# Kernel tuning notes

Measured on AMD Instinct MI355X. Metric: run time of the kernel, lower is better.

The kernel has to match this reference:

```python
import jax, jax.numpy as jnp
import numpy as np

B, N, K = 2, 2048, 30          # batch, residues, neighbors
DN, DE, L = 256, 128, 3        # dim_nodes, dim_edges, num_layers
NF, EF = 12, 28                # raw node / edge feature dims
EPS = 1e-6


def _gather(h, idx):
    # h: [B,N,D], idx: [B,N,K] -> [B,N,K,D]
    b, n, k = idx.shape
    d = h.shape[-1]
    return jnp.take_along_axis(h, idx.reshape(b, n * k, 1), axis=1).reshape(b, n, k, d)


def _nrm(v):
    return v / (jnp.linalg.norm(v, axis=-1, keepdims=True) + EPS)


def _forward(X, C, Wn, bn, We, be, Wm1, bm1, Wm2, bm2, Wue1, bue1, Wue2, bue2):
    mask_i = (C > 0).astype(X.dtype)                      # [B,N]
    Nat, CA, Cat, Oat = X[..., 0, :], X[..., 1, :], X[..., 2, :], X[..., 3, :]

    # local residue frames via Gram-Schmidt on (N, CA, C)
    u = _nrm(Cat - CA)
    v0 = Nat - CA
    v = _nrm(v0 - jnp.sum(v0 * u, -1, keepdims=True) * u)
    w = jnp.cross(u, v)
    R = jnp.stack([u, v, w], axis=-1)                     # [B,N,3,3]

    # node features: internal coords (unit bond vectors + log lengths)
    def bond_feat(bv):
        return jnp.concatenate([_nrm(bv), jnp.log(jnp.linalg.norm(bv, axis=-1, keepdims=True) + EPS)], -1)
    node_feat = jnp.concatenate([bond_feat(CA - Nat), bond_feat(Cat - CA), bond_feat(Oat - Cat)], -1)  # [B,N,12]
    node_h = (node_feat @ Wn + bn) * mask_i[..., None]

    # kNN graph on centroid distances (graph_distance_atom_type=-1)
    Xc = X.mean(axis=2)                                   # [B,N,3]
    D2 = jnp.sum((Xc[:, :, None] - Xc[:, None, :]) ** 2, -1)  # [B,N,N]
    BIG = 1e9
    D2 = D2 + BIG * (1.0 - mask_i)[:, None, :] + BIG * jnp.eye(N, dtype=X.dtype)[None]
    _, edge_idx = jax.lax.top_k(-D2, K)                   # [B,N,K]

    mask_j = _gather(mask_i[..., None], edge_idx)[..., 0]
    mask_ij = mask_i[..., None] * mask_j                  # [B,N,K]

    # edge features: RBF distances + local-frame direction + relative rotation
    xj = _gather(Xc, edge_idx)
    d = xj - Xc[:, :, None]                               # [B,N,K,3]
    dist = jnp.linalg.norm(d, axis=-1)
    local = jnp.einsum('bndc,bnkd->bnkc', R, d)           # R_i^T d
    dirv = local / (dist[..., None] + EPS)
    Rj = _gather(R.reshape(B, N, 9), edge_idx).reshape(B, N, K, 3, 3)
    Rrel = jnp.einsum('bnde,bnkdf->bnkef', R, Rj).reshape(B, N, K, 9)  # R_i^T R_j
    centers = jnp.linspace(0.0, 20.0, 16)
    sigma = 20.0 / 16.0
    rbf = jnp.exp(-(((dist[..., None] - centers) / sigma) ** 2))       # [B,N,K,16]
    edge_h = (jnp.concatenate([rbf, dirv, Rrel], -1) @ We + be) * mask_ij[..., None]

    # GNN message passing: gather -> MLP -> masked mean scatter, + edge update
    denom = jnp.sum(mask_ij, -1, keepdims=True) + EPS     # [B,N,1]
    for l in range(L):
        hj = _gather(node_h, edge_idx)                    # [B,N,K,DN]
        hi = jnp.broadcast_to(node_h[:, :, None], hj.shape)
        mi = jnp.concatenate([hi, hj, edge_h], -1)        # [B,N,K,2*DN+DE]
        m = jax.nn.softplus(mi @ Wm1[l] + bm1[l]) @ Wm2[l] + bm2[l]
        m = m * mask_ij[..., None]
        node_h = (node_h + m.sum(axis=2) / denom) * mask_i[..., None]
        e = jax.nn.softplus(mi @ Wue1[l] + bue1[l]) @ Wue2[l] + bue2[l]
        edge_h = (edge_h + e) * mask_ij[..., None]

    return node_h, edge_h, edge_idx, mask_i, mask_ij


def setup_inputs() -> dict:
    key = jax.random.key(0)
    ks = jax.random.split(key, 10)
    s = lambda i, shp: jax.random.normal(ks[i], shp, jnp.float32) * 0.05
    M = 2 * DN + DE
    inp = {
        'X': jax.random.normal(ks[0], (B, N, 4, 3), jnp.float32),
        'C': jax.random.randint(ks[1], (B, N), 0, 4),
        'Wn': s(2, (NF, DN)), 'bn': jnp.zeros((DN,), jnp.float32),
        'We': s(3, (EF, DE)), 'be': jnp.zeros((DE,), jnp.float32),
        'Wm1': s(4, (L, M, DN)), 'bm1': jnp.zeros((L, DN), jnp.float32),
        'Wm2': s(5, (L, DN, DN)), 'bm2': jnp.zeros((L, DN), jnp.float32),
        'Wue1': s(6, (L, M, DE)), 'bue1': jnp.zeros((L, DE), jnp.float32),
        'Wue2': s(7, (L, DE, DE)), 'bue2': jnp.zeros((L, DE), jnp.float32),
    }
    return inp


def reference(X, C, Wn, bn, We, be, Wm1, bm1, Wm2, bm2, Wue1, bue1, Wue2, bue2):
    return _forward(X, C, Wn, bn, We, be, Wm1, bm1, Wm2, bm2, Wue1, bue1, Wue2, bue2)
```

## Files before the change

kernel.cpp:

```cpp
#include <hip/hip_runtime.h>
#include <math.h>

#define Bdim 2
#define Nn   2048
#define Kn   30
#define KP   32
#define DNc  256
#define DEc  128
#define NODES (Bdim*Nn)
#define EDGES (Bdim*Nn*Kn)
#define RPAD  (NODES*KP)
#define EPSF 1e-6f

#define BK 64
#define LDA (BK+8)
#define LDP 136

typedef __attribute__((ext_vector_type(8))) short short8;
typedef __attribute__((ext_vector_type(4))) short sh4;
typedef __attribute__((ext_vector_type(4))) float floatx4;

__device__ __forceinline__ float softplusf(float x){
    float e = __expf(-fabsf(x));
    return fmaxf(x, 0.f) + __logf(1.f + e);
}

__device__ __forceinline__ unsigned short f2bf(float x){
    union { float f; unsigned u; } v; v.f = x;
    unsigned r = v.u + 0x7fff + ((v.u >> 16) & 1);
    return (unsigned short)(r >> 16);
}
__device__ __forceinline__ float bf2f(unsigned short h){
    union { unsigned u; float f; } v; v.u = ((unsigned)h) << 16;
    return v.f;
}

__global__ __launch_bounds__(256) void k_geom(
    const float* __restrict__ X, const int* __restrict__ C,
    float* __restrict__ Xc, float* __restrict__ Rm,
    float* __restrict__ feat, float* __restrict__ mask_out)
{
    int id = blockIdx.x*256 + threadIdx.x;
    if (id >= NODES) return;
    float a[4][3];
    #pragma unroll
    for (int t=0;t<4;++t)
        #pragma unroll
        for (int d=0;d<3;++d) a[t][d] = X[id*12 + t*3 + d];
    #pragma unroll
    for (int d=0; d<3; ++d){
        float s = __fadd_rn(__fadd_rn(__fadd_rn(a[0][d],a[1][d]),a[2][d]),a[3][d]);
        Xc[id*3+d] = __fmul_rn(s, 0.25f);
    }
    mask_out[id] = (C[id] > 0) ? 1.f : 0.f;

    float u[3], v[3], w[3], b2[3], v0[3], vv[3];
    #pragma unroll
    for (int d=0;d<3;++d) b2[d] = a[2][d]-a[1][d];
    float n2 = sqrtf(b2[0]*b2[0]+b2[1]*b2[1]+b2[2]*b2[2]);
    #pragma unroll
    for (int d=0;d<3;++d) u[d] = b2[d]/(n2+EPSF);
    #pragma unroll
    for (int d=0;d<3;++d) v0[d] = a[0][d]-a[1][d];
    float dt = v0[0]*u[0]+v0[1]*u[1]+v0[2]*u[2];
    #pragma unroll
    for (int d=0;d<3;++d) vv[d] = v0[d] - dt*u[d];
    float nv = sqrtf(vv[0]*vv[0]+vv[1]*vv[1]+vv[2]*vv[2]);
    #pragma unroll
    for (int d=0;d<3;++d) v[d] = vv[d]/(nv+EPSF);
    w[0] = u[1]*v[2]-u[2]*v[1];
    w[1] = u[2]*v[0]-u[0]*v[2];
    w[2] = u[0]*v[1]-u[1]*v[0];
    #pragma unroll
    for (int d=0;d<3;++d){
        Rm[id*9 + d*3 + 0] = u[d];
        Rm[id*9 + d*3 + 1] = v[d];
        Rm[id*9 + d*3 + 2] = w[d];
    }
    float bonds[3][3];
    #pragma unroll
    for (int d=0;d<3;++d){
        bonds[0][d] = a[1][d]-a[0][d];
        bonds[1][d] = b2[d];
        bonds[2][d] = a[3][d]-a[2][d];
    }
    #pragma unroll
    for (int bi=0;bi<3;++bi){
        float nb = sqrtf(bonds[bi][0]*bonds[bi][0]+bonds[bi][1]*bonds[bi][1]+bonds[bi][2]*bonds[bi][2]);
        #pragma unroll
        for (int d=0;d<3;++d) feat[id*12 + bi*4 + d] = bonds[bi][d]/(nb+EPSF);
        feat[id*12 + bi*4 + 3] = logf(nb+EPSF);
    }
}

__global__ __launch_bounds__(256) void k_nodeh(
    const float* __restrict__ feat, const float* __restrict__ Wn,
    const float* __restrict__ bn, const int* __restrict__ C,
    float* __restrict__ node_h, unsigned short* __restrict__ node_bf)
{
    int nid = blockIdx.x;
    int c   = threadIdx.x;
    __shared__ float f[12];
    if (c < 12) f[c] = feat[nid*12 + c];
    __syncthreads();
    float acc = bn[c];
    #pragma unroll
    for (int k=0;k<12;++k) acc += f[k]*Wn[k*DNc + c];
    float mask = (C[nid] > 0) ? 1.f : 0.f;
    float r = acc*mask;
    node_h[nid*DNc + c] = r;
    node_bf[nid*DNc + c] = f2bf(r);
}

__global__ __launch_bounds__(256) void k_knn(
    const float* __restrict__ Xc, const int* __restrict__ C,
    int* __restrict__ eidx, float* __restrict__ eidx_f)
{
    __shared__ float sx[Nn], sy[Nn], sz[Nn], sadd[Nn];
    int tid  = threadIdx.x;
    int lane = tid & 63, wave = tid >> 6;
    int node0 = blockIdx.x*4;
    int base  = (node0 >> 11) << 11;
    for (int j=tid; j<Nn; j+=256){
        int gj = base + j;
        sx[j] = Xc[gj*3+0]; sy[j] = Xc[gj*3+1]; sz[j] = Xc[gj*3+2];
        sadd[j] = (C[gj] > 0) ? 0.f : 1e9f;
    }
    __syncthreads();

    int node = node0 + wave;
    int iloc = node & (Nn-1);
    float xi = sx[iloc], yi = sy[iloc], zi = sz[iloc];

    unsigned long long kreg[32];
    unsigned long long gm[8];
    #pragma unroll
    for (int t=0; t<32; ++t){
        int j = lane + t*64;
        float dx = __fsub_rn(xi, sx[j]);
        float dy = __fsub_rn(yi, sy[j]);
        float dz = __fsub_rn(zi, sz[j]);
        float vv = __fadd_rn(__fadd_rn(__fmul_rn(dx,dx),__fmul_rn(dy,dy)),__fmul_rn(dz,dz));
        vv = __fadd_rn(vv, sadd[j]);
        if (j == iloc) vv = __fadd_rn(vv, 1e9f);
        union { float f; unsigned u; } cv; cv.f = vv;
        kreg[t] = (((unsigned long long)cv.u) << 11) | (unsigned)j;
    }
    #pragma unroll
    for (int g=0; g<8; ++g){
        unsigned long long a = kreg[4*g+0], b = kreg[4*g+1];
        unsigned long long c = kreg[4*g+2], d = kreg[4*g+3];
        unsigned long long m1 = a<b?a:b, m2 = c<d?c:d;
        gm[g] = m1<m2?m1:m2;
    }
    unsigned long long m = gm[0]; int marg = 0;
    #pragma unroll
    for (int g=1; g<8; ++g) if (gm[g] < m){ m = gm[g]; marg = g; }

    for (int kk=0; kk<Kn; ++kk){
        unsigned long long best = m;
        #pragma unroll
        for (int d=1; d<64; d<<=1){
            unsigned long long o = __shfl_xor(best, d, 64);
            if (o < best) best = o;
        }
        if (lane == 0){
            int j = (int)(best & 2047ull);
            eidx  [(size_t)node*Kn + kk] = j;
            eidx_f[(size_t)node*Kn + kk] = (float)j;
        }
        if (m == best){
            #pragma unroll
            for (int g=0; g<8; ++g){
                if (marg == g){
                    #pragma unroll
                    for (int t=0; t<4; ++t)
                        if (kreg[4*g+t] == best) kreg[4*g+t] = ~0ull;
                    unsigned long long a = kreg[4*g+0], b = kreg[4*g+1];
                    unsigned long long c = kreg[4*g+2], d = kreg[4*g+3];
                    unsigned long long m1 = a<b?a:b, m2 = c<d?c:d;
                    gm[g] = m1<m2?m1:m2;
                }
            }
            m = gm[0]; marg = 0;
            #pragma unroll
            for (int g=1; g<8; ++g) if (gm[g] < m){ m = gm[g]; marg = g; }
        }
    }
}

__global__ __launch_bounds__(256) void k_edge(
    const float* __restrict__ Xc, const float* __restrict__ Rm,
    const int* __restrict__ eidx, const int* __restrict__ C,
    const float* __restrict__ We, const float* __restrict__ be,
    unsigned short* __restrict__ edge_pad, float* __restrict__ mask_ij_out,
    float* __restrict__ mask_pad, int* __restrict__ jg_pad,
    float* __restrict__ cnt)
{
    __shared__ float sWe[28*128];
    __shared__ float sbe[128];
    __shared__ float sfeat[30][28];
    __shared__ float smij[30];
    __shared__ float sRi[9];
    int nid = blockIdx.x;
    int b   = nid >> 11;
    int tid = threadIdx.x;
    for (int idx=tid; idx<28*128; idx+=256) sWe[idx] = We[idx];
    if (tid < 128) sbe[tid] = be[tid];
    if (tid < 9)   sRi[tid] = Rm[nid*9 + tid];
    __syncthreads();
    if (tid < KP){
        if (tid < Kn){
            int e  = nid*Kn + tid;
            int j  = eidx[e];
            int jb = (b<<11) + j;
            jg_pad[nid*KP + tid] = jb;
            float d0 = Xc[jb*3+0]-Xc[nid*3+0];
            float d1 = Xc[jb*3+1]-Xc[nid*3+1];
            float d2v= Xc[jb*3+2]-Xc[nid*3+2];
            float dist = sqrtf(d0*d0+d1*d1+d2v*d2v);
            float mij = (C[nid] > 0 && C[jb] > 0) ? 1.f : 0.f;
            smij[tid] = mij;
            mask_ij_out[e] = mij;
            mask_pad[nid*KP + tid] = mij;
            #pragma unroll
            for (int c=0; c<16; ++c){
                float ctr = (20.f/15.f)*(float)c;
                float t = (dist - ctr)*(1.f/1.25f);
                sfeat[tid][c] = expf(-t*t);
            }
            #pragma unroll
            for (int cc=0; cc<3; ++cc){
                float loc = sRi[0*3+cc]*d0 + sRi[1*3+cc]*d1 + sRi[2*3+cc]*d2v;
                sfeat[tid][16+cc] = loc/(dist+EPSF);
            }
            float rj[9];
            #pragma unroll
            for (int q=0;q<9;++q) rj[q] = Rm[jb*9+q];
            #pragma unroll
            for (int ee=0; ee<3; ++ee)
                #pragma unroll
                for (int ff=0; ff<3; ++ff)
                    sfeat[tid][19+ee*3+ff] = sRi[0+ee]*rj[0+ff] + sRi[3+ee]*rj[3+ff] + sRi[6+ee]*rj[6+ff];
        } else {
            jg_pad[nid*KP + tid] = nid;
            mask_pad[nid*KP + tid] = 0.f;
        }
    }
    __syncthreads();
    if (tid == 0){
        float c = 0.f;
        #pragma unroll
        for (int k=0;k<Kn;++k) c += smij[k];
        cnt[nid] = c;
    }
    int c  = tid & 127;
    int eg = tid >> 7;
    for (int k=eg; k<KP; k+=2){
        if (k < Kn){
            float acc = sbe[c];
            #pragma unroll
            for (int f=0; f<28; ++f) acc += sfeat[k][f]*sWe[f*128 + c];
            edge_pad[(size_t)(nid*KP + k)*DEc + c] = f2bf(acc * smij[k]);
        } else {
            edge_pad[(size_t)(nid*KP + k)*DEc + c] = 0;
        }
    }
}

__global__ __launch_bounds__(256) void k_pack_pqw(
    const float* __restrict__ Wm1, const float* __restrict__ Wue1,
    unsigned short* __restrict__ wPQw)
{
    int id = blockIdx.x*256 + threadIdx.x;
    if (id >= 3*768*256) return;
    int l = id / (768*256);
    int rem = id % (768*256);
    int n = rem >> 8, k = rem & 255;
    int c = (n < 384) ? n : n - 384;
    int r = (n < 384) ? k : 256 + k;
    float v = (c < 256) ? Wm1[((size_t)l*640 + r)*256 + c]
                        : Wue1[((size_t)l*640 + r)*128 + (c-256)];
    wPQw[id] = f2bf(v);
}

__global__ __launch_bounds__(256) void k_pack_ew(
    const float* __restrict__ Wm1, const float* __restrict__ Wue1,
    unsigned short* __restrict__ wEw)
{
    int id = blockIdx.x*256 + threadIdx.x;
    if (id >= 3*384*128) return;
    int l = id / (384*128);
    int rem = id % (384*128);
    int n = rem >> 7, k = rem & 127;
    int r = 512 + k;
    float v = (n < 256) ? Wm1[((size_t)l*640 + r)*256 + n]
                        : Wue1[((size_t)l*640 + r)*128 + (n-256)];
    wEw[id] = f2bf(v);
}

__global__ __launch_bounds__(256) void k_pack_ue2(
    const float* __restrict__ Wue2, unsigned short* __restrict__ wUe2w)
{
    int id = blockIdx.x*256 + threadIdx.x;
    if (id >= 3*128*128) return;
    int l = id / (128*128);
    int rem = id % (128*128);
    int n = rem >> 7, k = rem & 127;
    wUe2w[id] = f2bf(Wue2[((size_t)l*128 + k)*128 + n]);
}

__global__ __launch_bounds__(256) void k_pack_m2(
    const float* __restrict__ Wm2, unsigned short* __restrict__ wM2w)
{
    int id = blockIdx.x*256 + threadIdx.x;
    if (id >= 3*256*256) return;
    int l = id / (256*256);
    int rem = id % (256*256);
    int n = rem >> 8, k = rem & 255;
    wM2w[id] = f2bf(Wm2[((size_t)l*256 + k)*256 + n]);
}

template<int NR>
__device__ __forceinline__ void stage_tile_t(
    const unsigned short* __restrict__ gbase, int ldg, int k0,
    unsigned short* lds, int tid)
{
    #pragma unroll
    for (int it=0; it<NR/32; ++it){
        int idx = it*256 + tid;
        int row = idx >> 3;
        int ke  = (idx & 7) * 8;
        const float4* src = (const float4*)(gbase + (size_t)row*ldg + k0 + ke);
        *(float4*)(&lds[row*LDA + ke]) = *src;
    }
}

template<int TI, int TJ>
__device__ __forceinline__ void mma_tile_t(
    const unsigned short* Als, const unsigned short* Bls,
    int wm, int wn, int lane, floatx4 acc[TI][TJ])
{
    #pragma unroll
    for (int s=0; s<2; ++s){
        short8 af[TI], bf[TJ];
        int kidx = s*32 + (lane>>4)*8;
        #pragma unroll
        for (int t=0;t<TI;++t){
            int row = wm*(TI*16) + t*16 + (lane&15);
            af[t] = *(const short8*)(&Als[row*LDA + kidx]);
        }
        #pragma unroll
        for (int t=0;t<TJ;++t){
            int col = wn*(TJ*16) + t*16 + (lane&15);
            bf[t] = *(const short8*)(&Bls[col*LDA + kidx]);
        }
        #pragma unroll
        for (int i=0;i<TI;++i)
            #pragma unroll
            for (int j=0;j<TJ;++j)
                acc[i][j] = __builtin_amdgcn_mfma_f32_16x16x32_bf16(af[i], bf[j], acc[i][j], 0,0,0);
    }
}

__device__ __forceinline__ void mma_tileA_lp(
    const unsigned short* Atile, const unsigned short* Bls,
    int k0, int wm, int wn, int lane, floatx4 acc[4][4])
{
    #pragma unroll
    for (int s=0; s<2; ++s){
        short8 af[4], bf[4];
        int kloc = s*32 + (lane>>4)*8;
        #pragma unroll
        for (int t=0;t<4;++t){
            int row = wm*64 + t*16 + (lane&15);
            af[t] = *(const short8*)(&Atile[row*LDP + k0 + kloc]);
            int col = wn*64 + t*16 + (lane&15);
            bf[t] = *(const short8*)(&Bls[col*LDA + kloc]);
        }
        #pragma unroll
        for (int i=0;i<4;++i)
            #pragma unroll
            for (int j=0;j<4;++j)
                acc[i][j] = __builtin_amdgcn_mfma_f32_16x16x32_bf16(af[i], bf[j], acc[i][j], 0,0,0);
    }
}

__global__ __launch_bounds__(256) void k_pq(
    const unsigned short* __restrict__ A, const unsigned short* __restrict__ Bw,
    unsigned short* __restrict__ PQbf,
    const float* __restrict__ bm1l, const float* __restrict__ bue1l)
{
    __shared__ __align__(16) unsigned short smem[(64+128)*LDA];
    unsigned short* Als = smem;
    unsigned short* Bls = smem + 64*LDA;
    unsigned short* tile = smem;
    int tid = threadIdx.x;
    int lane = tid & 63, wave = tid >> 6;
    int wm = wave >> 1, wn = wave & 1;
    const unsigned short* Ab = A + (size_t)blockIdx.x*64*256;
    const unsigned short* Bb = Bw + (size_t)blockIdx.y*128*256;
    floatx4 acc[2][4];
    #pragma unroll
    for (int i=0;i<2;++i)
        #pragma unroll
        for (int j=0;j<4;++j) acc[i][j] = (floatx4){0.f,0.f,0.f,0.f};
    for (int k0=0; k0<256; k0+=BK){
        stage_tile_t<64>(Ab, 256, k0, Als, tid);
        stage_tile_t<128>(Bb, 256, k0, Bls, tid);
        __syncthreads();
        mma_tile_t<2,4>(Als, Bls, wm, wn, lane, acc);
        __syncthreads();
    }
    int quad = lane >> 4, cl = lane & 15;
    #pragma unroll
    for (int i=0;i<2;++i){
        #pragma unroll
        for (int rg=0;rg<4;++rg){
            int rowl = wm*32 + i*16 + quad*4 + rg;
            #pragma unroll
            for (int j=0;j<4;++j){
                int coll = wn*64 + j*16 + cl;
                int col  = blockIdx.y*128 + coll;
                float biasv = 0.f;
                if (col < 256)       biasv = bm1l[col];
                else if (col < 384)  biasv = bue1l[col-256];
                tile[rowl*LDP + coll] = f2bf(acc[i][j][rg] + biasv);
            }
        }
    }
    __syncthreads();
    {
        int rl = tid >> 2;
        int h  = tid & 3;
        unsigned short* dst = PQbf + (size_t)(blockIdx.x*64 + rl)*768 + blockIdx.y*128 + h*32;
        #pragma unroll
        for (int q=0; q<4; ++q)
            *(short8*)(dst + q*8) = *(const short8*)(&tile[rl*LDP + h*32 + q*8]);
    }
}

__global__ __launch_bounds__(256) void k_h1s(
    const unsigned short* __restrict__ Apad, const unsigned short* __restrict__ Bw,
    const unsigned short* __restrict__ PQbf, const int* __restrict__ jg_pad,
    const float* __restrict__ mask_pad,
    unsigned short* __restrict__ Sout)
{
    __shared__ __align__(16) unsigned short smem[2*128*LDA];
    __shared__ float smask[128];
    unsigned short* Als = smem;
    unsigned short* Bls = smem + 128*LDA;
    unsigned short* pqT = smem;

    int tid = threadIdx.x;
    int lane = tid & 63, wave = tid >> 6;
    int wm = wave >> 1, wn = wave & 1;
    int colblk = blockIdx.y;

    const unsigned short* Ab = Apad + (size_t)blockIdx.x*128*128;
    const unsigned short* Bb = Bw + (size_t)colblk*128*128;
    floatx4 acc[4][4];
    #pragma unroll
    for (int i=0;i<4;++i)
        #pragma unroll
        for (int j=0;j<4;++j) acc[i][j] = (floatx4){0.f,0.f,0.f,0.f};
    for (int k0=0; k0<128; k0+=BK){
        stage_tile_t<128>(Ab, 128, k0, Als, tid);
        stage_tile_t<128>(Bb, 128, k0, Bls, tid);
        __syncthreads();
        mma_tile_t<4,4>(Als, Bls, wm, wn, lane, acc);
        __syncthreads();
    }

    {
        int colbase = colblk*128;
        #pragma unroll
        for (int it=0; it<2; ++it){
            int w    = it*256 + tid;
            int rq   = w & 31;
            int c8   = w >> 5;
            int row0 = rq*4;
            int r0   = blockIdx.x*128 + row0;
            int ni   = r0 >> 5;
            int4 jg4 = *(const int4*)&jg_pad[r0];
            int colg = colbase + c8*8;
            short8 pv = *(const short8*)(PQbf + (size_t)ni*768 + colg);
            short8 q0 = *(const short8*)(PQbf + (size_t)jg4.x*768 + 384 + colg);
            short8 q1 = *(const short8*)(PQbf + (size_t)jg4.y*768 + 384 + colg);
            short8 q2 = *(const short8*)(PQbf + (size_t)jg4.z*768 + 384 + colg);
            short8 q3 = *(const short8*)(PQbf + (size_t)jg4.w*768 + 384 + colg);
            #pragma unroll
            for (int q=0; q<8; ++q){
                float pf = bf2f((unsigned short)pv[q]);
                sh4 ov;
                ov[0] = (short)f2bf(pf + bf2f((unsigned short)q0[q]));
                ov[1] = (short)f2bf(pf + bf2f((unsigned short)q1[q]));
                ov[2] = (short)f2bf(pf + bf2f((unsigned short)q2[q]));
                ov[3] = (short)f2bf(pf + bf2f((unsigned short)q3[q]));
                *(sh4*)(&pqT[(c8*8 + q)*LDP + row0]) = ov;
            }
        }
        if (tid < 128) smask[tid] = mask_pad[blockIdx.x*128 + tid];
    }
    __syncthreads();

    int quad = lane >> 4, cl = lane & 15;
    float sumA[4] = {0.f,0.f,0.f,0.f};
    float sumB[4] = {0.f,0.f,0.f,0.f};
    #pragma unroll
    for (int i=0;i<4;++i){
        int rowl0 = wm*64 + i*16 + quad*4;
        float4 mk = *(const float4*)&smask[rowl0];
        float mkv[4] = {mk.x, mk.y, mk.z, mk.w};
        #pragma unroll
        for (int j=0;j<4;++j){
            int coll = wn*64 + j*16 + cl;
            sh4 pq4 = *(const sh4*)(&pqT[coll*LDP + rowl0]);
            #pragma unroll
            for (int rg=0; rg<4; ++rg){
                float v  = softplusf(acc[i][j][rg] + bf2f((unsigned short)pq4[rg]));
                float mv = mkv[rg]*v;
                if (i < 2) sumA[j] += mv; else sumB[j] += mv;
            }
        }
    }

    int nodeA = blockIdx.x*4 + wm*2;
    #pragma unroll
    for (int j=0;j<4;++j){
        float a = sumA[j];
        a += __shfl_xor(a, 16, 64);
        a += __shfl_xor(a, 32, 64);
        float b = sumB[j];
        b += __shfl_xor(b, 16, 64);
        b += __shfl_xor(b, 32, 64);
        int col = colblk*128 + wn*64 + j*16 + cl;
        if (quad == 0)      Sout[(size_t)nodeA*256 + col]     = f2bf(a);
        else if (quad == 1) Sout[(size_t)(nodeA+1)*256 + col] = f2bf(b);
    }
}

__global__ __launch_bounds__(256) void k_h1e(
    const unsigned short* __restrict__ Apad, const unsigned short* __restrict__ BwE,
    const unsigned short* __restrict__ BwU2,
    const unsigned short* __restrict__ PQbf, const int* __restrict__ jg_pad,
    const float* __restrict__ mask_pad, const float* __restrict__ bue2l,
    unsigned short* __restrict__ edge_pad, float* __restrict__ edge_f32,
    int last)
{
    __shared__ __align__(16) unsigned short smem[26624];
    unsigned short* Als  = smem;
    unsigned short* Bls  = smem + 128*LDA;
    unsigned short* tile = smem;
    unsigned short* B2   = smem + 128*LDP;

    int tid = threadIdx.x;
    int lane = tid & 63, wave = tid >> 6;
    int wm = wave >> 1, wn = wave & 1;

    const unsigned short* Ab = Apad + (size_t)blockIdx.x*128*128;
    floatx4 acc[4][4];
    #pragma unroll
    for (int i=0;i<4;++i)
        #pragma unroll
        for (int j=0;j<4;++j) acc[i][j] = (floatx4){0.f,0.f,0.f,0.f};
    for (int k0=0; k0<128; k0+=BK){
        stage_tile_t<128>(Ab, 128, k0, Als, tid);
        stage_tile_t<128>(BwE, 128, k0, Bls, tid);
        __syncthreads();
        mma_tile_t<4,4>(Als, Bls, wm, wn, lane, acc);
        __syncthreads();
    }

    stage_tile_t<128>(BwU2, 128, 0, B2, tid);

    {
        int rl = tid >> 1;
        int h  = tid & 1;
        int r  = blockIdx.x*128 + rl;
        int ni = r >> 5;
        int jg = jg_pad[r];
        int cb = 256 + h*64;
        const unsigned short* Pr = PQbf + (size_t)ni*768 + cb;
        const unsigned short* Qr = PQbf + (size_t)jg*768 + 384 + cb;
        #pragma unroll
        for (int q=0; q<8; ++q){
            short8 pv = *(const short8*)(Pr + q*8);
            short8 qv = *(const short8*)(Qr + q*8);
            short8 ov;
            #pragma unroll
            for (int z=0; z<8; ++z)
                ov[z] = (short)f2bf(bf2f((unsigned short)pv[z]) + bf2f((unsigned short)qv[z]));
            *(short8*)(&tile[rl*LDP + h*64 + q*8]) = ov;
        }
    }
    __syncthreads();

    int quad = lane >> 4, cl = lane & 15;
    #pragma unroll
    for (int i=0;i<4;++i){
        #pragma unroll
        for (int rg=0;rg<4;++rg){
            int rowl = wm*64 + i*16 + quad*4 + rg;
            #pragma unroll
            for (int j=0;j<4;++j){
                int coll = wn*64 + j*16 + cl;
                float pq = bf2f(tile[rowl*LDP + coll]);
                float v  = softplusf(acc[i][j][rg] + pq);
                tile[rowl*LDP + coll] = f2bf(v);
            }
        }
    }
    __syncthreads();

    floatx4 acc2[4][4];
    #pragma unroll
    for (int i=0;i<4;++i)
        #pragma unroll
        for (int j=0;j<4;++j) acc2[i][j] = (floatx4){0.f,0.f,0.f,0.f};
    mma_tileA_lp(tile, B2, 0, wm, wn, lane, acc2);
    __syncthreads();
    stage_tile_t<128>(BwU2, 128, 64, B2, tid);
    __syncthreads();
    mma_tileA_lp(tile, B2, 64, wm, wn, lane, acc2);
    __syncthreads();

    float* sbias = (float*)B2;
    #pragma unroll
    for (int i=0;i<4;++i){
        #pragma unroll
        for (int rg=0;rg<4;++rg){
            int rowl = wm*64 + i*16 + quad*4 + rg;
            #pragma unroll
            for (int j=0;j<4;++j){
                int coll = wn*64 + j*16 + cl;
                tile[rowl*LDP + coll] = f2bf(acc2[i][j][rg]);
            }
        }
    }
    if (tid < 128) sbias[tid] = bue2l[tid];
    __syncthreads();

    if (last){
        int c16  = lane & 31;
        int rsub = lane >> 5;
        #pragma unroll
        for (int step=0; step<16; ++step){
            int rowl = wave*32 + step*2 + rsub;
            int R = blockIdx.x*128 + rowl;
            int k = R & (KP-1);
            if (k < Kn){
                float mij = mask_pad[R];
                int node = R >> 5;
                int e = node*Kn + k;
                sh4 ov = *(const sh4*)(edge_pad + (size_t)R*128 + c16*4);
                sh4 av = *(const sh4*)(&tile[rowl*LDP + c16*4]);
                float4 bv = *(const float4*)(&sbias[c16*4]);
                float4 f;
                f.x = (bf2f((unsigned short)ov[0]) + bf2f((unsigned short)av[0]) + bv.x)*mij;
                f.y = (bf2f((unsigned short)ov[1]) + bf2f((unsigned short)av[1]) + bv.y)*mij;
                f.z = (bf2f((unsigned short)ov[2]) + bf2f((unsigned short)av[2]) + bv.z)*mij;
                f.w = (bf2f((unsigned short)ov[3]) + bf2f((unsigned short)av[3]) + bv.w)*mij;
                *(float4*)(edge_f32 + (size_t)e*128 + c16*4) = f;
            }
        }
    } else {
        int c8   = lane & 15;
        int rsub = lane >> 4;
        #pragma unroll
        for (int step=0; step<8; ++step){
            int rowl = wave*32 + step*4 + rsub;
            int R = blockIdx.x*128 + rowl;
            int k = R & (KP-1);
            if (k < Kn){
                float mij = mask_pad[R];
                unsigned short* ep = edge_pad + (size_t)R*128 + c8*8;
                short8 ov = *(const short8*)ep;
                short8 av = *(const short8*)(&tile[rowl*LDP + c8*8]);
                float4 b0 = *(const float4*)(&sbias[c8*8]);
                float4 b1 = *(const float4*)(&sbias[c8*8 + 4]);
                float nv[8];
                nv[0] = (bf2f((unsigned short)ov[0]) + bf2f((unsigned short)av[0]) + b0.x)*mij;
                nv[1] = (bf2f((unsigned short)ov[1]) + bf2f((unsigned short)av[1]) + b0.y)*mij;
                nv[2] = (bf2f((unsigned short)ov[2]) + bf2f((unsigned short)av[2]) + b0.z)*mij;
                nv[3] = (bf2f((unsigned short)ov[3]) + bf2f((unsigned short)av[3]) + b0.w)*mij;
                nv[4] = (bf2f((unsigned short)ov[4]) + bf2f((unsigned short)av[4]) + b1.x)*mij;
                nv[5] = (bf2f((unsigned short)ov[5]) + bf2f((unsigned short)av[5]) + b1.y)*mij;
                nv[6] = (bf2f((unsigned short)ov[6]) + bf2f((unsigned short)av[6]) + b1.z)*mij;
                nv[7] = (bf2f((unsigned short)ov[7]) + bf2f((unsigned short)av[7]) + b1.w)*mij;
                short8 sv;
                #pragma unroll
                for (int z=0; z<8; ++z) sv[z] = (short)f2bf(nv[z]);
                *(short8*)ep = sv;
            }
        }
    }
}

__global__ __launch_bounds__(256) void k_node_gemm(
    const unsigned short* __restrict__ S, const unsigned short* __restrict__ Bw,
    const float* __restrict__ bm2l, const float* __restrict__ cnt,
    const float* __restrict__ mask_i,
    float* __restrict__ node_h, unsigned short* __restrict__ node_bf)
{
    __shared__ __align__(16) unsigned short Als[64*LDA];
    __shared__ __align__(16) unsigned short Bls[64*LDA];
    int tid = threadIdx.x;
    int lane = tid & 63, wave = tid >> 6;
    int wm = wave >> 1, wn = wave & 1;
    const unsigned short* Ab = S + (size_t)blockIdx.x*64*256;
    const unsigned short* Bb = Bw + (size_t)blockIdx.y*64*256;
    floatx4 acc[2][2];
    #pragma unroll
    for (int i=0;i<2;++i)
        #pragma unroll
        for (int j=0;j<2;++j) acc[i][j] = (floatx4){0.f,0.f,0.f,0.f};
    for (int k0=0; k0<256; k0+=BK){
        stage_tile_t<64>(Ab, 256, k0, Als, tid);
        stage_tile_t<64>(Bb, 256, k0, Bls, tid);
        __syncthreads();
        mma_tile_t<2,2>(Als, Bls, wm, wn, lane, acc);
        __syncthreads();
    }
    int quad = lane >> 4, cl = lane & 15;
    #pragma unroll
    for (int i=0;i<2;++i){
        #pragma unroll
        for (int rg=0;rg<4;++rg){
            int nid = blockIdx.x*64 + wm*32 + i*16 + quad*4 + rg;
            float ct = cnt[nid];
            float mi = mask_i[nid];
            #pragma unroll
            for (int j=0;j<2;++j){
                int col = blockIdx.y*64 + wn*32 + j*16 + cl;
                float msum = acc[i][j][rg] + ct*bm2l[col];
                float nh = node_h[(size_t)nid*256 + col];
                float r = (nh + msum/(ct+EPSF))*mi;
                node_h[(size_t)nid*256 + col] = r;
                node_bf[(size_t)nid*256 + col] = f2bf(r);
            }
        }
    }
}

extern "C" void kernel_launch(void* const* d_in, const int* in_sizes, int n_in,
                              void* d_out, int out_size, void* d_ws, size_t ws_size,
                              hipStream_t stream)
{
    (void)in_sizes; (void)n_in; (void)out_size; (void)ws_size;
    const float* X   = (const float*)d_in[0];
    const int*   C   = (const int*)  d_in[1];
    const float* Wn  = (const float*)d_in[2];
    const float* bn  = (const float*)d_in[3];
    const float* We  = (const float*)d_in[4];
    const float* be  = (const float*)d_in[5];
    const float* Wm1 = (const float*)d_in[6];
    const float* bm1 = (const float*)d_in[7];
    const float* Wm2 = (const float*)d_in[8];
    const float* bm2 = (const float*)d_in[9];
    const float* Wue1= (const float*)d_in[10];
    const float* bue1= (const float*)d_in[11];
    const float* Wue2= (const float*)d_in[12];
    const float* bue2= (const float*)d_in[13];

    float* out       = (float*)d_out;
    float* out_node  = out;
    float* out_edge  = out + 1048576;
    float* out_eidxf = out + 16777216;
    float* out_maski = out + 16900096;
    float* out_maskij= out + 16904192;

    char* wsb = (char*)d_ws;
    size_t off = 0;
    float* wXc    = (float*)(wsb + off); off += (size_t)12288*4;
    float* wR     = (float*)(wsb + off); off += (size_t)36864*4;
    float* wF     = (float*)(wsb + off); off += (size_t)49152*4;
    int*   wEidx  = (int*)  (wsb + off); off += (size_t)EDGES*4;
    int*   wJgPad = (int*)  (wsb + off); off += (size_t)RPAD*4;
    float* wMaskP = (float*)(wsb + off); off += (size_t)RPAD*4;
    float* wCnt   = (float*)(wsb + off); off += (size_t)NODES*4;
    unsigned short* wPQ      = (unsigned short*)(wsb + off); off += (size_t)NODES*768*2;
    unsigned short* wS       = (unsigned short*)(wsb + off); off += (size_t)NODES*256*2;
    unsigned short* wNodeBf  = (unsigned short*)(wsb + off); off += (size_t)NODES*256*2;
    unsigned short* wEdgePad = (unsigned short*)(wsb + off); off += (size_t)RPAD*128*2;
    unsigned short* wPQw     = (unsigned short*)(wsb + off); off += (size_t)3*768*256*2;
    unsigned short* wEw      = (unsigned short*)(wsb + off); off += (size_t)3*384*128*2;
    unsigned short* wUe2w    = (unsigned short*)(wsb + off); off += (size_t)3*128*128*2;
    unsigned short* wM2w     = (unsigned short*)(wsb + off); off += (size_t)3*256*256*2;

    k_geom <<<16,    256, 0, stream>>>(X, C, wXc, wR, wF, out_maski);
    k_nodeh<<<NODES, 256, 0, stream>>>(wF, Wn, bn, C, out_node, wNodeBf);
    k_knn  <<<NODES/4, 256, 0, stream>>>(wXc, C, wEidx, out_eidxf);
    k_edge <<<NODES, 256, 0, stream>>>(wXc, wR, wEidx, C, We, be,
                                       wEdgePad, out_maskij, wMaskP, wJgPad, wCnt);

    k_pack_pqw<<<(3*768*256+255)/256, 256, 0, stream>>>(Wm1, Wue1, wPQw);
    k_pack_ew <<<(3*384*128+255)/256, 256, 0, stream>>>(Wm1, Wue1, wEw);
    k_pack_ue2<<<(3*128*128+255)/256, 256, 0, stream>>>(Wue2, wUe2w);
    k_pack_m2 <<<(3*256*256+255)/256, 256, 0, stream>>>(Wm2, wM2w);

    for (int l=0; l<3; ++l){
        k_pq<<<dim3(64,6), 256, 0, stream>>>(wNodeBf, wPQw + (size_t)l*768*256, wPQ,
                                             bm1 + l*256, bue1 + l*128);
        k_h1s<<<dim3(RPAD/128,2), 256, 0, stream>>>(
            wEdgePad, wEw + (size_t)l*384*128, wPQ, wJgPad, wMaskP, wS);
        k_h1e<<<RPAD/128, 256, 0, stream>>>(
            wEdgePad, wEw + (size_t)l*384*128 + (size_t)256*128,
            wUe2w + (size_t)l*128*128, wPQ, wJgPad, wMaskP, bue2 + l*128,
            wEdgePad, out_edge, (l==2) ? 1 : 0);
        k_node_gemm<<<dim3(NODES/64,4), 256, 0, stream>>>(
            wS, wM2w + (size_t)l*256*256, bm2 + l*256, wCnt, out_maski,
            out_node, wNodeBf);
    }
}
```

Before: 509.7 us.

## Split edge embedding into per-edge feature kernel and bf16 MFMA GEMM

```diff
diff --git a/kernel.cpp b/kernel.cpp
--- a/kernel.cpp
+++ b/kernel.cpp
@@ -14,6 +14,7 @@
 
 #define BK 64
 #define LDA (BK+8)
+#define LDA0 40
 #define LDP 136
 
 typedef __attribute__((ext_vector_type(8))) short short8;
@@ -189,83 +190,169 @@
     }
 }
 
-__global__ __launch_bounds__(256) void k_edge(
+__global__ __launch_bounds__(256) void k_edge_feat(
     const float* __restrict__ Xc, const float* __restrict__ Rm,
     const int* __restrict__ eidx, const int* __restrict__ C,
-    const float* __restrict__ We, const float* __restrict__ be,
-    unsigned short* __restrict__ edge_pad, float* __restrict__ mask_ij_out,
-    float* __restrict__ mask_pad, int* __restrict__ jg_pad,
-    float* __restrict__ cnt)
-{
-    __shared__ float sWe[28*128];
-    __shared__ float sbe[128];
-    __shared__ float sfeat[30][28];
-    __shared__ float smij[30];
-    __shared__ float sRi[9];
-    int nid = blockIdx.x;
+    unsigned short* __restrict__ featp,
+    float* __restrict__ mask_ij_out, float* __restrict__ mask_pad,
+    int* __restrict__ jg_pad, float* __restrict__ cnt)
+{
+    int r   = blockIdx.x*256 + threadIdx.x;
+    int nid = r >> 5;
+    int k   = r & 31;
     int b   = nid >> 11;
+    float mij = 0.f;
+    int   jb  = nid;
+    float f[28];
+    if (k < Kn){
+        int e = nid*Kn + k;
+        int j = eidx[e];
+        jb = (b<<11) + j;
+        mij = (C[nid] > 0 && C[jb] > 0) ? 1.f : 0.f;
+        mask_ij_out[e] = mij;
+        float xi0 = Xc[nid*3+0], xi1 = Xc[nid*3+1], xi2 = Xc[nid*3+2];
+        float d0  = Xc[jb*3+0]-xi0;
+        float d1  = Xc[jb*3+1]-xi1;
+        float d2v = Xc[jb*3+2]-xi2;
+        float dist = sqrtf(d0*d0 + d1*d1 + d2v*d2v);
+        float ri[9], rj[9];
+        #pragma unroll
+        for (int q=0;q<9;++q) ri[q] = Rm[nid*9+q];
+        #pragma unroll
+        for (int q=0;q<9;++q) rj[q] = Rm[jb*9+q];
+        #pragma unroll
+        for (int c=0; c<16; ++c){
+            float ctr = (20.f/15.f)*(float)c;
+            float t = (dist - ctr)*(1.f/1.25f);
+            f[c] = expf(-t*t);
+        }
+        #pragma unroll
+        for (int cc=0; cc<3; ++cc){
+            float loc = ri[0*3+cc]*d0 + ri[1*3+cc]*d1 + ri[2*3+cc]*d2v;
+            f[16+cc] = loc/(dist+EPSF);
+        }
+        #pragma unroll
+        for (int ee=0; ee<3; ++ee)
+            #pragma unroll
+            for (int ff=0; ff<3; ++ff)
+                f[19+ee*3+ff] = ri[0+ee]*rj[0+ff] + ri[3+ee]*rj[3+ff] + ri[6+ee]*rj[6+ff];
+    }
+    jg_pad[r]   = jb;
+    mask_pad[r] = mij;
+
+    unsigned long long bal = __ballot(mij > 0.f);
+    int lane = threadIdx.x & 63;
+    if (lane == 0)  cnt[r >> 5] = (float)__popcll(bal & 0xFFFFFFFFull);
+    if (lane == 32) cnt[r >> 5] = (float)__popcll(bal >> 32);
+
+    unsigned short ov[32];
+    #pragma unroll
+    for (int q=0;q<32;++q) ov[q] = 0;
+    if (k < Kn){
+        #pragma unroll
+        for (int q=0;q<28;++q) ov[q] = f2bf(f[q]);
+    }
+    unsigned short* dst = featp + (size_t)r*32;
+    #pragma unroll
+    for (int q=0; q<4; ++q){
+        short8 sv;
+        #pragma unroll
+        for (int z=0; z<8; ++z) sv[z] = (short)ov[q*8+z];
+        *(short8*)(dst + q*8) = sv;
+    }
+}
+
+__global__ __launch_bounds__(256) void k_edge0(
+    const unsigned short* __restrict__ featp, const unsigned short* __restrict__ Wp,
+    const float* __restrict__ be, const float* __restrict__ mask_pad,
+    unsigned short* __restrict__ edge_pad)
+{
+    __shared__ __align__(16) unsigned short smem[128*LDP];
+    __shared__ float smask[128];
+    unsigned short* Als  = smem;
+    unsigned short* Bls  = smem + 128*LDA0;
+    unsigned short* tile = smem;
+
     int tid = threadIdx.x;
-    for (int idx=tid; idx<28*128; idx+=256) sWe[idx] = We[idx];
-    if (tid < 128) sbe[tid] = be[tid];
-    if (tid < 9)   sRi[tid] = Rm[nid*9 + tid];
-    __syncthreads();
-    if (tid < KP){
-        if (tid < Kn){
-            int e  = nid*Kn + tid;
-            int j  = eidx[e];
-            int jb = (b<<11) + j;
-            jg_pad[nid*KP + tid] = jb;
-            float d0 = Xc[jb*3+0]-Xc[nid*3+0];
-            float d1 = Xc[jb*3+1]-Xc[nid*3+1];
-            float d2v= Xc[jb*3+2]-Xc[nid*3+2];
-            float dist = sqrtf(d0*d0+d1*d1+d2v*d2v);
-            float mij = (C[nid] > 0 && C[jb] > 0) ? 1.f : 0.f;
-            smij[tid] = mij;
-            mask_ij_out[e] = mij;
-            mask_pad[nid*KP + tid] = mij;
-            #pragma unroll
-            for (int c=0; c<16; ++c){
-                float ctr = (20.f/15.f)*(float)c;
-                float t = (dist - ctr)*(1.f/1.25f);
-                sfeat[tid][c] = expf(-t*t);
+    int lane = tid & 63, wave = tid >> 6;
+    int wm = wave >> 1, wn = wave & 1;
+
+    {
+        const unsigned short* Ab = featp + (size_t)blockIdx.x*128*32;
+        #pragma unroll
+        for (int it=0; it<2; ++it){
+            int idx = it*256 + tid;
+            int row = idx >> 2, q = idx & 3;
+            *(float4*)(&Als[row*LDA0 + q*8]) = *(const float4*)(Ab + row*32 + q*8);
+        }
+        if (tid < 128){
+            int row = tid;
+            *(float4*)(&Bls[row*LDA0 + 0])  = *(const float4*)(Wp + row*32 + 0);
+            *(float4*)(&Bls[row*LDA0 + 8])  = *(const float4*)(Wp + row*32 + 8);
+            *(float4*)(&Bls[row*LDA0 + 16]) = *(const float4*)(Wp + row*32 + 16);
+            *(float4*)(&Bls[row*LDA0 + 24]) = *(const float4*)(Wp + row*32 + 24);
+        } else {
+            smask[tid-128] = mask_pad[blockIdx.x*128 + (tid-128)];
+        }
+    }
+    __syncthreads();
+
+    floatx4 acc[4][4];
+    #pragma unroll
+    for (int i=0;i<4;++i)
+        #pragma unroll
+        for (int j=0;j<4;++j) acc[i][j] = (floatx4){0.f,0.f,0.f,0.f};
+    short8 af[4], bf[4];
+    int kidx = (lane>>4)*8;
+    #pragma unroll
+    for (int t=0;t<4;++t){
+        int row = wm*64 + t*16 + (lane&15);
+        af[t] = *(const short8*)(&Als[row*LDA0 + kidx]);
+        int col = wn*64 + t*16 + (lane&15);
+        bf[t] = *(const short8*)(&Bls[col*LDA0 + kidx]);
+    }
+    __syncthreads();
+    #pragma unroll
+    for (int i=0;i<4;++i)
+        #pragma unroll
+        for (int j=0;j<4;++j)
+            acc[i][j] = __builtin_amdgcn_mfma_f32_16x16x32_bf16(af[i], bf[j], acc[i][j], 0,0,0);
+
+    int quad = lane >> 4, cl = lane & 15;
+    float be_r[4];
+    #pragma unroll
+    for (int j=0;j<4;++j) be_r[j] = be[wn*64 + j*16 + cl];
+    #pragma unroll
+    for (int i=0;i<4;++i){
+        #pragma unroll
+        for (int rg=0;rg<4;++rg){
+            int rowl = wm*64 + i*16 + quad*4 + rg;
+            float mk = smask[rowl];
+            #pragma unroll
+            for (int j=0;j<4;++j){
+                int coll = wn*64 + j*16 + cl;
+                tile[rowl*LDP + coll] = f2bf((acc[i][j][rg] + be_r[j]) * mk);
             }
-            #pragma unroll
-            for (int cc=0; cc<3; ++cc){
-                float loc = sRi[0*3+cc]*d0 + sRi[1*3+cc]*d1 + sRi[2*3+cc]*d2v;
-                sfeat[tid][16+cc] = loc/(dist+EPSF);
-            }
-            float rj[9];
-            #pragma unroll
-            for (int q=0;q<9;++q) rj[q] = Rm[jb*9+q];
-            #pragma unroll
-            for (int ee=0; ee<3; ++ee)
-                #pragma unroll
-                for (int ff=0; ff<3; ++ff)
-                    sfeat[tid][19+ee*3+ff] = sRi[0+ee]*rj[0+ff] + sRi[3+ee]*rj[3+ff] + sRi[6+ee]*rj[6+ff];
-        } else {
-            jg_pad[nid*KP + tid] = nid;
-            mask_pad[nid*KP + tid] = 0.f;
-        }
-    }
-    __syncthreads();
-    if (tid == 0){
-        float c = 0.f;
-        #pragma unroll
-        for (int k=0;k<Kn;++k) c += smij[k];
-        cnt[nid] = c;
-    }
-    int c  = tid & 127;
-    int eg = tid >> 7;
-    for (int k=eg; k<KP; k+=2){
-        if (k < Kn){
-            float acc = sbe[c];
-            #pragma unroll
-            for (int f=0; f<28; ++f) acc += sfeat[k][f]*sWe[f*128 + c];
-            edge_pad[(size_t)(nid*KP + k)*DEc + c] = f2bf(acc * smij[k]);
-        } else {
-            edge_pad[(size_t)(nid*KP + k)*DEc + c] = 0;
-        }
-    }
+        }
+    }
+    __syncthreads();
+    {
+        int rl = tid >> 1;
+        int h  = tid & 1;
+        unsigned short* dst = edge_pad + (size_t)(blockIdx.x*128 + rl)*128 + h*64;
+        #pragma unroll
+        for (int q=0; q<8; ++q)
+            *(short8*)(dst + q*8) = *(const short8*)(&tile[rl*LDP + h*64 + q*8]);
+    }
+}
+
+__global__ __launch_bounds__(256) void k_pack_we0(
+    const float* __restrict__ We, unsigned short* __restrict__ Wp)
+{
+    int id = blockIdx.x*256 + threadIdx.x;
+    if (id >= 128*32) return;
+    int n = id >> 5, kk = id & 31;
+    Wp[id] = (kk < 28) ? f2bf(We[kk*128 + n]) : 0;
 }
 
 __global__ __launch_bounds__(256) void k_pack_pqw(
@@ -783,6 +870,8 @@
     unsigned short* wS       = (unsigned short*)(wsb + off); off += (size_t)NODES*256*2;
     unsigned short* wNodeBf  = (unsigned short*)(wsb + off); off += (size_t)NODES*256*2;
     unsigned short* wEdgePad = (unsigned short*)(wsb + off); off += (size_t)RPAD*128*2;
+    unsigned short* wFeatP   = (unsigned short*)(wsb + off); off += (size_t)RPAD*32*2;
+    unsigned short* wWe0     = (unsigned short*)(wsb + off); off += (size_t)128*32*2;
     unsigned short* wPQw     = (unsigned short*)(wsb + off); off += (size_t)3*768*256*2;
     unsigned short* wEw      = (unsigned short*)(wsb + off); off += (size_t)3*384*128*2;
     unsigned short* wUe2w    = (unsigned short*)(wsb + off); off += (size_t)3*128*128*2;
@@ -791,8 +880,11 @@
     k_geom <<<16,    256, 0, stream>>>(X, C, wXc, wR, wF, out_maski);
     k_nodeh<<<NODES, 256, 0, stream>>>(wF, Wn, bn, C, out_node, wNodeBf);
     k_knn  <<<NODES/4, 256, 0, stream>>>(wXc, C, wEidx, out_eidxf);
-    k_edge <<<NODES, 256, 0, stream>>>(wXc, wR, wEidx, C, We, be,
-                                       wEdgePad, out_maskij, wMaskP, wJgPad, wCnt);
+
+    k_pack_we0<<<16, 256, 0, stream>>>(We, wWe0);
+    k_edge_feat<<<RPAD/256, 256, 0, stream>>>(wXc, wR, wEidx, C, wFeatP,
+                                              out_maskij, wMaskP, wJgPad, wCnt);
+    k_edge0<<<RPAD/128, 256, 0, stream>>>(wFeatP, wWe0, be, wMaskP, wEdgePad);
 
     k_pack_pqw<<<(3*768*256+255)/256, 256, 0, stream>>>(Wm1, Wue1, wPQw);
     k_pack_ew <<<(3*384*128+255)/256, 256, 0, stream>>>(Wm1, Wue1, wEw);
```

New measurement: 484.9 us. 1.05x faster.
